# Performance work log

Hardware: AMD Instinct MI355X
Metric: run time of the kernel (lower is better)

Reference implementation:

```python
import jax, jax.numpy as jnp
import numpy as np

NUM_EXPERTS = 64
TOPK = 2  # moe_router_topk


def setup_inputs() -> dict:
    key = jax.random.key(0)
    k1, k2 = jax.random.split(key)
    # [seq, batch, hidden] as in Megatron
    hidden_states = jax.random.normal(k1, (2048, 4, 4096), dtype=jnp.float32)
    # gating weight: Linear(hidden -> num_experts), no bias
    router_weight = jax.random.normal(k2, (NUM_EXPERTS, 4096), dtype=jnp.float32) * 0.02
    return {"hidden_states": hidden_states, "router_weight": router_weight}


def reference(hidden_states, router_weight):
    S, B, H = hidden_states.shape
    x = hidden_states.reshape(-1, H)  # [T, H], T = S*B tokens
    # Router gating is always done in fp32 in Megatron.
    logits = jnp.einsum('th,eh->te', x.astype(jnp.float32),
                        router_weight.astype(jnp.float32))  # [T, E]
    # top-k routing (moe_router_pre_softmax=False): top-k over logits,
    # then softmax over the selected k logits.
    top_vals, top_idx = jax.lax.top_k(logits, TOPK)        # [T, k]
    top_probs = jax.nn.softmax(top_vals, axis=-1)          # [T, k]
    T, E = logits.shape
    rows = jnp.arange(T)[:, None]                          # [T, 1]
    # dense probs: selected probs scattered back, zeros elsewhere
    probs = jnp.zeros((T, E), dtype=logits.dtype).at[rows, top_idx].set(top_probs)
    # boolean routing map [T, E]
    routing_map = jnp.zeros((T, E), dtype=bool).at[rows, top_idx].set(True)
    return probs, routing_map
```

## Files before the change

### kernel.cpp

```cpp
#include <hip/hip_runtime.h>
#include <math.h>


#define HDIM 4096
#define NEXP 64
#define NTOK 8192
#define HG 8
#define HSLAB (HDIM / HG)
#define NCHUNK (HSLAB / 64)
#define TPB 64

__global__ void wtrans_kernel(const float* __restrict__ W, float* __restrict__ Wt) {
    __shared__ float tile[64][65];
    int h0 = blockIdx.x * 64;
    int lx = threadIdx.x & 63;
    int ly = threadIdx.x >> 6;
    #pragma unroll
    for (int p = 0; p < 16; ++p) {
        int e = p * 4 + ly;
        tile[lx][e] = W[(size_t)e * HDIM + h0 + lx];
    }
    __syncthreads();
    #pragma unroll
    for (int p = 0; p < 16; ++p) {
        int hh = p * 4 + ly;
        Wt[(size_t)(h0 + hh) * NEXP + lx] = tile[hh][lx];
    }
}

__global__ __launch_bounds__(256, 4) void logits_kernel(
        const float* __restrict__ X, const float* __restrict__ Wt,
        float* __restrict__ part) {
    const int tg   = blockIdx.x >> 3;
    const int hg   = blockIdx.x & 7;
    const int lane = threadIdx.x & 63;
    const int wave = __builtin_amdgcn_readfirstlane((int)(threadIdx.x >> 6));

    __shared__ float smem[4 * 64 * 33];
    float (*xs)[65]      = reinterpret_cast<float(*)[65]>(smem);
    float (*buf)[64][33] = reinterpret_cast<float(*)[64][33]>(smem);

    const int token0 = tg * TPB;
    const int hbase  = hg * HSLAB;

    float acc[NEXP];
    #pragma unroll
    for (int e = 0; e < NEXP; ++e) acc[e] = 0.f;

    const float* Xblk = X + (size_t)token0 * HDIM + hbase;
    const int r4 = threadIdx.x >> 4;
    const int f4 = threadIdx.x & 15;

    for (int c = 0; c < NCHUNK; ++c) {
        __syncthreads();
        #pragma unroll
        for (int q = 0; q < 4; ++q) {
            int r = q * 16 + r4;
            float4 v = *reinterpret_cast<const float4*>(
                Xblk + (size_t)r * HDIM + c * 64 + f4 * 4);
            xs[r][f4 * 4 + 0] = v.x;
            xs[r][f4 * 4 + 1] = v.y;
            xs[r][f4 * 4 + 2] = v.z;
            xs[r][f4 * 4 + 3] = v.w;
        }
        __syncthreads();
        const float* wrow = Wt + (size_t)(hbase + c * 64 + wave * 16) * NEXP;
        #pragma unroll
        for (int j = 0; j < 16; ++j) {
            float xv = xs[lane][wave * 16 + j];
            const float* w = wrow + (size_t)j * NEXP;
            #pragma unroll
            for (int e = 0; e < NEXP; ++e)
                acc[e] = fmaf(xv, w[e], acc[e]);
        }
    }

    #pragma unroll
    for (int cc = 0; cc < 2; ++cc) {
        __syncthreads();
        #pragma unroll
        for (int i = 0; i < 32; ++i) buf[wave][lane][i] = acc[cc * 32 + i];
        __syncthreads();
        int ec = threadIdx.x & 31;
        int t0 = threadIdx.x >> 5;
        #pragma unroll
        for (int p = 0; p < 8; ++p) {
            int t = p * 8 + t0;
            float s = buf[0][t][ec] + buf[1][t][ec] + buf[2][t][ec] + buf[3][t][ec];
            part[((size_t)hg * NTOK + (size_t)tg * TPB + t) * NEXP + cc * 32 + ec] = s;
        }
    }
}

__global__ __launch_bounds__(256) void topk_kernel(
        const float* __restrict__ part, float* __restrict__ probs,
        float* __restrict__ rmap) {
    const int wave = threadIdx.x >> 6;
    const int lane = threadIdx.x & 63;
    const int token = blockIdx.x * 4 + wave;

    const float* p = part + (size_t)token * NEXP + lane;
    float v = 0.f;
    #pragma unroll
    for (int hg = 0; hg < HG; ++hg) v += p[(size_t)hg * NTOK * NEXP];

    float m1 = v; int i1 = lane;
    #pragma unroll
    for (int s = 32; s > 0; s >>= 1) {
        float om = __shfl_xor(m1, s, 64);
        int   oi = __shfl_xor(i1, s, 64);
        if (om > m1 || (om == m1 && oi < i1)) { m1 = om; i1 = oi; }
    }
    float vx = (lane == i1) ? -INFINITY : v;
    float m2 = vx; int i2 = lane;
    #pragma unroll
    for (int s = 32; s > 0; s >>= 1) {
        float om = __shfl_xor(m2, s, 64);
        int   oi = __shfl_xor(i2, s, 64);
        if (om > m2 || (om == m2 && oi < i2)) { m2 = om; i2 = oi; }
    }

    float e2 = expf(m2 - m1);
    float p1 = 1.f / (1.f + e2);
    float p2 = 1.f - p1;

    float prob = (lane == i1) ? p1 : ((lane == i2) ? p2 : 0.f);
    float flag = (lane == i1 || lane == i2) ? 1.f : 0.f;
    probs[(size_t)token * NEXP + lane] = prob;
    rmap [(size_t)token * NEXP + lane] = flag;
}

extern "C" void kernel_launch(void* const* d_in, const int* in_sizes, int n_in,
                              void* d_out, int out_size, void* d_ws, size_t ws_size,
                              hipStream_t stream) {
    const float* X = (const float*)d_in[0];
    const float* W = (const float*)d_in[1];
    float* out   = (float*)d_out;
    float* Wt    = (float*)d_ws;
    float* part  = Wt + (size_t)HDIM * NEXP;

    wtrans_kernel<<<HDIM / 64, 256, 0, stream>>>(W, Wt);
    logits_kernel<<<128 * HG, 256, 0, stream>>>(X, Wt, part);
    topk_kernel<<<NTOK / 4, 256, 0, stream>>>(part, out, out + (size_t)NTOK * NEXP);
}
```

Before: 228.2 us.

## Compute two tokens per thread and double-buffer X tiles with register prefetch

```diff
diff --git a/kernel.cpp b/kernel.cpp
--- a/kernel.cpp
+++ b/kernel.cpp
@@ -8,7 +8,8 @@
 #define HG 8
 #define HSLAB (HDIM / HG)
 #define NCHUNK (HSLAB / 64)
-#define TPB 64
+#define TPB 128
+#define XSTRIDE 65
 
 __global__ void wtrans_kernel(const float* __restrict__ W, float* __restrict__ Wt) {
     __shared__ float tile[64][65];
@@ -28,7 +29,7 @@
     }
 }
 
-__global__ __launch_bounds__(256, 4) void logits_kernel(
+__global__ __launch_bounds__(256, 2) void logits_kernel(
         const float* __restrict__ X, const float* __restrict__ Wt,
         float* __restrict__ part) {
     const int tg   = blockIdx.x >> 3;
@@ -36,58 +37,88 @@
     const int lane = threadIdx.x & 63;
     const int wave = __builtin_amdgcn_readfirstlane((int)(threadIdx.x >> 6));
 
-    __shared__ float smem[4 * 64 * 33];
-    float (*xs)[65]      = reinterpret_cast<float(*)[65]>(smem);
-    float (*buf)[64][33] = reinterpret_cast<float(*)[64][33]>(smem);
+    __shared__ float smem[2 * TPB * XSTRIDE];
+    float* xs0 = smem;
+    float* xs1 = smem + TPB * XSTRIDE;
+    float (*red)[TPB][17] = reinterpret_cast<float(*)[TPB][17]>(smem);
 
     const int token0 = tg * TPB;
     const int hbase  = hg * HSLAB;
 
-    float acc[NEXP];
+    float acc0[NEXP], acc1[NEXP];
     #pragma unroll
-    for (int e = 0; e < NEXP; ++e) acc[e] = 0.f;
+    for (int e = 0; e < NEXP; ++e) { acc0[e] = 0.f; acc1[e] = 0.f; }
 
     const float* Xblk = X + (size_t)token0 * HDIM + hbase;
     const int r4 = threadIdx.x >> 4;
     const int f4 = threadIdx.x & 15;
 
+    float4 pf[8];
+    #pragma unroll
+    for (int q = 0; q < 8; ++q) {
+        int r = q * 16 + r4;
+        pf[q] = *reinterpret_cast<const float4*>(Xblk + (size_t)r * HDIM + f4 * 4);
+    }
+    #pragma unroll
+    for (int q = 0; q < 8; ++q) {
+        int r = q * 16 + r4;
+        float* dst = xs0 + r * XSTRIDE + f4 * 4;
+        dst[0] = pf[q].x; dst[1] = pf[q].y; dst[2] = pf[q].z; dst[3] = pf[q].w;
+    }
+    __syncthreads();
+
+    const int xoff = lane * XSTRIDE + wave * 16;
+
     for (int c = 0; c < NCHUNK; ++c) {
-        __syncthreads();
-        #pragma unroll
-        for (int q = 0; q < 4; ++q) {
-            int r = q * 16 + r4;
-            float4 v = *reinterpret_cast<const float4*>(
-                Xblk + (size_t)r * HDIM + c * 64 + f4 * 4);
-            xs[r][f4 * 4 + 0] = v.x;
-            xs[r][f4 * 4 + 1] = v.y;
-            xs[r][f4 * 4 + 2] = v.z;
-            xs[r][f4 * 4 + 3] = v.w;
+        float* cur = (c & 1) ? xs1 : xs0;
+        float* nxt = (c & 1) ? xs0 : xs1;
+        if (c + 1 < NCHUNK) {
+            #pragma unroll
+            for (int q = 0; q < 8; ++q) {
+                int r = q * 16 + r4;
+                pf[q] = *reinterpret_cast<const float4*>(
+                    Xblk + (size_t)r * HDIM + (c + 1) * 64 + f4 * 4);
+            }
         }
-        __syncthreads();
         const float* wrow = Wt + (size_t)(hbase + c * 64 + wave * 16) * NEXP;
         #pragma unroll
         for (int j = 0; j < 16; ++j) {
-            float xv = xs[lane][wave * 16 + j];
+            float x0 = cur[xoff + j];
+            float x1 = cur[xoff + 64 * XSTRIDE + j];
             const float* w = wrow + (size_t)j * NEXP;
             #pragma unroll
-            for (int e = 0; e < NEXP; ++e)
-                acc[e] = fmaf(xv, w[e], acc[e]);
+            for (int e = 0; e < NEXP; ++e) {
+                acc0[e] = fmaf(x0, w[e], acc0[e]);
+                acc1[e] = fmaf(x1, w[e], acc1[e]);
+            }
         }
+        if (c + 1 < NCHUNK) {
+            #pragma unroll
+            for (int q = 0; q < 8; ++q) {
+                int r = q * 16 + r4;
+                float* dst = nxt + r * XSTRIDE + f4 * 4;
+                dst[0] = pf[q].x; dst[1] = pf[q].y; dst[2] = pf[q].z; dst[3] = pf[q].w;
+            }
+        }
+        __syncthreads();
     }
 
+    const int ec = threadIdx.x & 15;
+    const int tq = threadIdx.x >> 4;
     #pragma unroll
-    for (int cc = 0; cc < 2; ++cc) {
+    for (int ce = 0; ce < 4; ++ce) {
         __syncthreads();
         #pragma unroll
-        for (int i = 0; i < 32; ++i) buf[wave][lane][i] = acc[cc * 32 + i];
+        for (int i = 0; i < 16; ++i) {
+            red[wave][lane][i]      = acc0[ce * 16 + i];
+            red[wave][lane + 64][i] = acc1[ce * 16 + i];
+        }
         __syncthreads();
-        int ec = threadIdx.x & 31;
-        int t0 = threadIdx.x >> 5;
         #pragma unroll
         for (int p = 0; p < 8; ++p) {
-            int t = p * 8 + t0;
-            float s = buf[0][t][ec] + buf[1][t][ec] + buf[2][t][ec] + buf[3][t][ec];
-            part[((size_t)hg * NTOK + (size_t)tg * TPB + t) * NEXP + cc * 32 + ec] = s;
+            int t = p * 16 + tq;
+            float s = red[0][t][ec] + red[1][t][ec] + red[2][t][ec] + red[3][t][ec];
+            part[((size_t)hg * NTOK + token0 + t) * NEXP + ce * 16 + ec] = s;
         }
     }
 }
@@ -140,6 +171,6 @@
     float* part  = Wt + (size_t)HDIM * NEXP;
 
     wtrans_kernel<<<HDIM / 64, 256, 0, stream>>>(W, Wt);
-    logits_kernel<<<128 * HG, 256, 0, stream>>>(X, Wt, part);
+    logits_kernel<<<64 * HG, 256, 0, stream>>>(X, Wt, part);
     topk_kernel<<<NTOK / 4, 256, 0, stream>>>(part, out, out + (size_t)NTOK * NEXP);
 }
```

Result: slower. 354.0 us (+55.1%).
